# Performance work log

Measured on AMD Instinct MI355X. Metric: run time of the kernel, lower is better.

The kernel has to match this reference:

```python
import jax, jax.numpy as jnp
import numpy as np

GRID_SIZE = 5
GRID_LO, GRID_HI = -1.0, 1.0


def setup_inputs() -> dict:
    key = jax.random.key(0)
    k1, k2 = jax.random.split(key)
    B, out_dim, in_dim, H, W = 8, 64, 64, 192, 192
    G = GRID_SIZE + 1
    x = jax.random.normal(k1, (B, in_dim, H, W), dtype=jnp.float32)
    coef = jax.random.normal(k2, (B, out_dim, in_dim, G), dtype=jnp.float32) * 0.1
    return {"x": x, "coef": coef}


def reference(x, coef):
    # x: [B, in_dim, H, W]; coef: [B, out_dim, in_dim, G] with G = grid_size + 1
    G = GRID_SIZE + 1
    grid = jnp.linspace(GRID_LO, GRID_HI, G, dtype=x.dtype)
    lo, hi = grid[0], grid[-1]
    spacing = grid[1] - grid[0]

    B, in_dim, H, W = x.shape
    out_dim = coef.shape[1]
    P = H * W

    xf = x.reshape(B, in_dim, P)
    xc = jnp.clip(xf, lo, hi)
    nx = (xc - lo) / spacing                      # normalized coordinate in [0, grid_size]
    idx = jnp.clip(jnp.floor(nx).astype(jnp.int32), 0, GRID_SIZE - 1)  # left knot
    frac = nx - idx.astype(x.dtype)               # fractional offset (grad flows via nx)
    w1 = 1.0 - frac
    w2 = frac
    idx_next = jnp.clip(idx + 1, 0, GRID_SIZE)    # right knot (max index = G-1)

    # Two-hot interpolation weights over the G grid points: [B, in, P, G]
    Wt = (w1[..., None] * jax.nn.one_hot(idx, G, dtype=x.dtype)
          + w2[..., None] * jax.nn.one_hot(idx_next, G, dtype=x.dtype))

    # result[b,o,p] = sum_i sum_g Wt[b,i,p,g] * coef[b,o,i,g]
    out = jnp.einsum('bipg,boig->bop', Wt, coef)
    return out.reshape(B, out_dim, H, W)
```

## Files before the change

kernel.cpp:

```cpp
#include <hip/hip_runtime.h>
#include <stdint.h>


typedef __fp16 half8_t __attribute__((ext_vector_type(8)));
typedef __fp16 half2_t __attribute__((ext_vector_type(2)));
typedef float f32x4 __attribute__((ext_vector_type(4)));

#define NBATCH 8
#define OD 64
#define ID 64
#define PIX 36864
#define NG 6
#define PT 192
#define KI 16
#define NCHUNK 4
#define KC (KI * NG)
#define AROW 392
#define PTILES (PIX / PT)

__global__ __launch_bounds__(256, 3)
void kan_mfma(const float* __restrict__ x, const float* __restrict__ coef,
              float* __restrict__ out) {
  const int t = threadIdx.x;
  const int lane = t & 63;
  const int wave = t >> 6;
  const int q8 = lane >> 4;
  const int col = lane & 15;

  const int bid = blockIdx.x;
  const int b = bid / PTILES;
  const int ptile = bid % PTILES;
  const int p0 = ptile * PT;

  __shared__ __fp16 A_lds[OD][AROW] __attribute__((aligned(16)));

  {
    const int o = t >> 2;
    const int c = t & 3;
    const float* crow = coef + (size_t)b * (OD * ID * NG) + o * (ID * NG) + c * KC;
    __fp16* arow = &A_lds[o][c * KC];
#pragma unroll
    for (int blk = 0; blk < 8; ++blk) {
      f32x4 va = ((const f32x4*)crow)[blk * 3 + 0];
      f32x4 vb = ((const f32x4*)crow)[blk * 3 + 1];
      f32x4 vc = ((const f32x4*)crow)[blk * 3 + 2];
      const float lo[NG] = {va[0], va[1], va[2], va[3], vb[0], vb[1]};
      const float hi[NG] = {vb[2], vb[3], vc[0], vc[1], vc[2], vc[3]};
#pragma unroll
      for (int g = 0; g < NG; ++g) {
        half2_t h2 = __builtin_amdgcn_cvt_pkrtz(lo[g], hi[g]);
        *(half2_t*)&arow[g * KI + blk * 2] = h2;
      }
    }
  }

  f32x4 acc[4][3];
#pragma unroll
  for (int i = 0; i < 4; ++i)
#pragma unroll
    for (int j = 0; j < 3; ++j)
      acc[i][j] = (f32x4){0.f, 0.f, 0.f, 0.f};

  __syncthreads();

  const int iof0 = (q8 & 1) * 8;
  const int ghalf = q8 >> 1;
  const float* xb = x + (size_t)b * ID * PIX + p0 + wave * 48 + col
                      + (size_t)iof0 * PIX;

#pragma unroll
  for (int c = 0; c < NCHUNK; ++c) {
    const float* xs = xb + (size_t)(c * KI) * PIX;
    float nxv[3][8];
#pragma unroll
    for (int j = 0; j < 8; ++j) {
      const float* xj = xs + (size_t)j * PIX;
      float a0 = xj[0];
      float a1 = xj[16];
      float a2 = xj[32];
      nxv[0][j] = (fminf(fmaxf(a0, -1.f), 1.f) + 1.f) * 2.5f;
      nxv[1][j] = (fminf(fmaxf(a1, -1.f), 1.f) + 1.f) * 2.5f;
      nxv[2][j] = (fminf(fmaxf(a2, -1.f), 1.f) + 1.f) * 2.5f;
    }

#pragma unroll
    for (int ks = 0; ks < 3; ++ks) {
      half8_t af[4];
#pragma unroll
      for (int ot = 0; ot < 4; ++ot)
        af[ot] = *(const half8_t*)&A_lds[ot * 16 + col][c * KC + ks * 32 + q8 * 8];

      const float gf = (float)(2 * ks + ghalf);
#pragma unroll
      for (int pti = 0; pti < 3; ++pti) {
        union { half2_t h2[4]; half8_t v; } bu;
#pragma unroll
        for (int jj = 0; jj < 4; ++jj) {
          float h0 = fmaxf(0.f, 1.f - fabsf(nxv[pti][2 * jj] - gf));
          float h1 = fmaxf(0.f, 1.f - fabsf(nxv[pti][2 * jj + 1] - gf));
          bu.h2[jj] = __builtin_amdgcn_cvt_pkrtz(h0, h1);
        }
#pragma unroll
        for (int ot = 0; ot < 4; ++ot)
          acc[ot][pti] = __builtin_amdgcn_mfma_f32_16x16x32_f16(
              af[ot], bu.v, acc[ot][pti], 0, 0, 0);
      }
    }
  }

  float* ob = out + (size_t)b * OD * PIX + p0;
#pragma unroll
  for (int ot = 0; ot < 4; ++ot) {
#pragma unroll
    for (int pti = 0; pti < 3; ++pti) {
      int p = wave * 48 + pti * 16 + col;
#pragma unroll
      for (int r = 0; r < 4; ++r) {
        int o = ot * 16 + q8 * 4 + r;
        __builtin_nontemporal_store(acc[ot][pti][r], &ob[(size_t)o * PIX + p]);
      }
    }
  }
}

extern "C" void kernel_launch(void* const* d_in, const int* in_sizes, int n_in,
                              void* d_out, int out_size, void* d_ws, size_t ws_size,
                              hipStream_t stream) {
  const float* x = (const float*)d_in[0];
  const float* coef = (const float*)d_in[1];
  float* out = (float*)d_out;
  dim3 grid(NBATCH * PTILES);
  dim3 block(256);
  hipLaunchKernelGGL(kan_mfma, grid, block, 0, stream, x, coef, out);
}
```

Measured before the change: 161.2 us.

## Double-buffer x loads with inline asm and issue first chunk before coef staging

Issues the global loads for the first input chunk before the coefficient-to-LDS staging, then double-buffers the following chunks in registers using inline-asm loads and explicit vmcnt waits. The intent is to hide global-memory latency behind the LDS fill and the MFMA work. It also folds the clamp and normalize into one fma plus clamp, moves the hat-function max to a packed half2 max after conversion, and replaces nontemporal output stores with normal stores. The extra 48 registers per thread for the two buffers may put pressure on the 3-blocks-per-CU occupancy target.

Result: faster. 152.0 us (-5.7%).

```diff
diff --git a/kernel.cpp b/kernel.cpp
--- a/kernel.cpp
+++ b/kernel.cpp
@@ -18,6 +18,26 @@
 #define AROW 392
 #define PTILES (PIX / PT)
 
+#define LOADCHUNK(dst, cc)                                                      \
+  do {                                                                          \
+    _Pragma("unroll") for (int j = 0; j < 8; ++j) {                             \
+      const float* a_ = xb + (size_t)((cc) * KI + j) * PIX;                     \
+      asm volatile("global_load_dword %0, %3, off\n\t"                          \
+                   "global_load_dword %1, %3, off offset:64\n\t"                \
+                   "global_load_dword %2, %3, off offset:128"                   \
+                   : "=&v"(dst[j * 3 + 0]), "=&v"(dst[j * 3 + 1]),              \
+                     "=&v"(dst[j * 3 + 2])                                      \
+                   : "v"(a_));                                                  \
+    }                                                                           \
+    __builtin_amdgcn_sched_barrier(0);                                          \
+  } while (0)
+
+#define VMWAIT(n)                                                               \
+  do {                                                                          \
+    asm volatile("s_waitcnt vmcnt(" #n ")" ::: "memory");                       \
+    __builtin_amdgcn_sched_barrier(0);                                          \
+  } while (0)
+
 __global__ __launch_bounds__(256, 3)
 void kan_mfma(const float* __restrict__ x, const float* __restrict__ coef,
               float* __restrict__ out) {
@@ -33,6 +53,15 @@
   const int p0 = ptile * PT;
 
   __shared__ __fp16 A_lds[OD][AROW] __attribute__((aligned(16)));
+
+  const int iof0 = (q8 & 1) * 8;
+  const int ghalf = q8 >> 1;
+  const float* xb = x + (size_t)b * ID * PIX + p0 + wave * 48 + col
+                      + (size_t)iof0 * PIX;
+
+  float xA[24], xB[24];
+
+  LOADCHUNK(xA, 0);
 
   {
     const int o = t >> 2;
@@ -63,24 +92,24 @@
 
   __syncthreads();
 
-  const int iof0 = (q8 & 1) * 8;
-  const int ghalf = q8 >> 1;
-  const float* xb = x + (size_t)b * ID * PIX + p0 + wave * 48 + col
-                      + (size_t)iof0 * PIX;
-
 #pragma unroll
   for (int c = 0; c < NCHUNK; ++c) {
-    const float* xs = xb + (size_t)(c * KI) * PIX;
+    float* xc = (c & 1) ? xB : xA;
+    float* xn = (c & 1) ? xA : xB;
+
+    if (c + 1 < NCHUNK) {
+      LOADCHUNK(xn, c + 1);
+      VMWAIT(24);
+    } else {
+      VMWAIT(0);
+    }
+
     float nxv[3][8];
 #pragma unroll
     for (int j = 0; j < 8; ++j) {
-      const float* xj = xs + (size_t)j * PIX;
-      float a0 = xj[0];
-      float a1 = xj[16];
-      float a2 = xj[32];
-      nxv[0][j] = (fminf(fmaxf(a0, -1.f), 1.f) + 1.f) * 2.5f;
-      nxv[1][j] = (fminf(fmaxf(a1, -1.f), 1.f) + 1.f) * 2.5f;
-      nxv[2][j] = (fminf(fmaxf(a2, -1.f), 1.f) + 1.f) * 2.5f;
+#pragma unroll
+      for (int pt = 0; pt < 3; ++pt)
+        nxv[pt][j] = fminf(fmaxf(xc[j * 3 + pt] * 2.5f + 2.5f, 0.f), 5.f);
     }
 
 #pragma unroll
@@ -96,9 +125,10 @@
         union { half2_t h2[4]; half8_t v; } bu;
 #pragma unroll
         for (int jj = 0; jj < 4; ++jj) {
-          float h0 = fmaxf(0.f, 1.f - fabsf(nxv[pti][2 * jj] - gf));
-          float h1 = fmaxf(0.f, 1.f - fabsf(nxv[pti][2 * jj + 1] - gf));
-          bu.h2[jj] = __builtin_amdgcn_cvt_pkrtz(h0, h1);
+          float h0 = 1.f - fabsf(nxv[pti][2 * jj] - gf);
+          float h1 = 1.f - fabsf(nxv[pti][2 * jj + 1] - gf);
+          half2_t h2 = __builtin_amdgcn_cvt_pkrtz(h0, h1);
+          bu.h2[jj] = __builtin_elementwise_max(h2, (half2_t)(__fp16)0.f);
         }
 #pragma unroll
         for (int ot = 0; ot < 4; ++ot)
@@ -117,7 +147,7 @@
 #pragma unroll
       for (int r = 0; r < 4; ++r) {
         int o = ot * 16 + q8 * 4 + r;
-        __builtin_nontemporal_store(acc[ot][pti][r], &ob[(size_t)o * PIX + p]);
+        ob[(size_t)o * PIX + p] = acc[ot][pti][r];
       }
     }
   }
```

## Stage fp16 normalized inputs and output tile through LDS with vector accesses

Applied to the files above, without the earlier changes.

Each block now loads its x tile with coalesced float4 reads and converts it once to clamped normalized coordinates. These are packed as fp16 pairs into an LDS table that all waves read, replacing the strided per-lane scalar global loads and repeated normalization. The hat weights are computed with packed half2 arithmetic instead of fp32 followed by conversion. The output tile is staged through LDS, reusing the coefficient buffer, so stores are written as coalesced float4 nontemporal stores. Occupancy drops to two blocks per CU, extra barriers are added, and fp16 coordinates lower interpolation precision.

Result: faster. 149.6 us (-7.2%).

```diff
diff --git a/kernel.cpp b/kernel.cpp
--- a/kernel.cpp
+++ b/kernel.cpp
@@ -5,6 +5,7 @@
 typedef __fp16 half8_t __attribute__((ext_vector_type(8)));
 typedef __fp16 half2_t __attribute__((ext_vector_type(2)));
 typedef float f32x4 __attribute__((ext_vector_type(4)));
+typedef uint32_t u32x4 __attribute__((ext_vector_type(4)));
 
 #define NBATCH 8
 #define OD 64
@@ -16,9 +17,11 @@
 #define NCHUNK 4
 #define KC (KI * NG)
 #define AROW 392
+#define XSTR 196
+#define SROW 196
 #define PTILES (PIX / PT)
 
-__global__ __launch_bounds__(256, 3)
+__global__ __launch_bounds__(256, 2)
 void kan_mfma(const float* __restrict__ x, const float* __restrict__ coef,
               float* __restrict__ out) {
   const int t = threadIdx.x;
@@ -33,6 +36,15 @@
   const int p0 = ptile * PT;
 
   __shared__ __fp16 A_lds[OD][AROW] __attribute__((aligned(16)));
+  __shared__ uint32_t NX[2 * KI][XSTR] __attribute__((aligned(16)));
+
+  f32x4 xrow[16];
+  const float* xbase = x + (size_t)b * ID * PIX + p0;
+  if (lane < 48) {
+#pragma unroll
+    for (int k = 0; k < 16; ++k)
+      xrow[k] = *(const f32x4*)(xbase + (size_t)(wave * 16 + k) * PIX + lane * 4);
+  }
 
   {
     const int o = t >> 2;
@@ -54,6 +66,22 @@
     }
   }
 
+  if (lane < 48) {
+#pragma unroll
+    for (int pr = 0; pr < 8; ++pr) {
+      u32x4 w4;
+#pragma unroll
+      for (int j = 0; j < 4; ++j) {
+        float e = fminf(fmaxf(xrow[2 * pr][j] * 2.5f + 2.5f, 0.f), 5.f);
+        float o = fminf(fmaxf(xrow[2 * pr + 1][j] * 2.5f + 2.5f, 0.f), 5.f);
+        union { half2_t h; uint32_t u; } cv;
+        cv.h = __builtin_amdgcn_cvt_pkrtz(e, o);
+        w4[j] = cv.u;
+      }
+      *(u32x4*)&NX[wave * 8 + pr][lane * 4] = w4;
+    }
+  }
+
   f32x4 acc[4][3];
 #pragma unroll
   for (int i = 0; i < 4; ++i)
@@ -63,25 +91,20 @@
 
   __syncthreads();
 
-  const int iof0 = (q8 & 1) * 8;
   const int ghalf = q8 >> 1;
-  const float* xb = x + (size_t)b * ID * PIX + p0 + wave * 48 + col
-                      + (size_t)iof0 * PIX;
+  const int ipof = (q8 & 1) * 4;
+  const int wp = wave * 48 + col;
+  const half2_t one2 = {(__fp16)1.f, (__fp16)1.f};
+  const half2_t zero2 = {(__fp16)0.f, (__fp16)0.f};
 
 #pragma unroll
   for (int c = 0; c < NCHUNK; ++c) {
-    const float* xs = xb + (size_t)(c * KI) * PIX;
-    float nxv[3][8];
+    uint32_t nxp[3][4];
 #pragma unroll
-    for (int j = 0; j < 8; ++j) {
-      const float* xj = xs + (size_t)j * PIX;
-      float a0 = xj[0];
-      float a1 = xj[16];
-      float a2 = xj[32];
-      nxv[0][j] = (fminf(fmaxf(a0, -1.f), 1.f) + 1.f) * 2.5f;
-      nxv[1][j] = (fminf(fmaxf(a1, -1.f), 1.f) + 1.f) * 2.5f;
-      nxv[2][j] = (fminf(fmaxf(a2, -1.f), 1.f) + 1.f) * 2.5f;
-    }
+    for (int pti = 0; pti < 3; ++pti)
+#pragma unroll
+      for (int jj = 0; jj < 4; ++jj)
+        nxp[pti][jj] = NX[c * 8 + ipof + jj][wp + pti * 16];
 
 #pragma unroll
     for (int ks = 0; ks < 3; ++ks) {
@@ -90,15 +113,21 @@
       for (int ot = 0; ot < 4; ++ot)
         af[ot] = *(const half8_t*)&A_lds[ot * 16 + col][c * KC + ks * 32 + q8 * 8];
 
-      const float gf = (float)(2 * ks + ghalf);
+      const __fp16 gh = (__fp16)(float)(2 * ks + ghalf);
+      const half2_t gf2 = {gh, gh};
 #pragma unroll
       for (int pti = 0; pti < 3; ++pti) {
         union { half2_t h2[4]; half8_t v; } bu;
 #pragma unroll
         for (int jj = 0; jj < 4; ++jj) {
-          float h0 = fmaxf(0.f, 1.f - fabsf(nxv[pti][2 * jj] - gf));
-          float h1 = fmaxf(0.f, 1.f - fabsf(nxv[pti][2 * jj + 1] - gf));
-          bu.h2[jj] = __builtin_amdgcn_cvt_pkrtz(h0, h1);
+          union { uint32_t u; half2_t h; } nx;
+          nx.u = nxp[pti][jj];
+          half2_t d = nx.h - gf2;
+          union { half2_t h; uint32_t u; } du;
+          du.h = d;
+          du.u &= 0x7FFF7FFFu;
+          half2_t hh = one2 - du.h;
+          bu.h2[jj] = __builtin_elementwise_max(hh, zero2);
         }
 #pragma unroll
         for (int ot = 0; ot < 4; ++ot)
@@ -108,7 +137,8 @@
     }
   }
 
-  float* ob = out + (size_t)b * OD * PIX + p0;
+  __syncthreads();
+  float* S = (float*)&A_lds[0][0];
 #pragma unroll
   for (int ot = 0; ot < 4; ++ot) {
 #pragma unroll
@@ -117,8 +147,21 @@
 #pragma unroll
       for (int r = 0; r < 4; ++r) {
         int o = ot * 16 + q8 * 4 + r;
-        __builtin_nontemporal_store(acc[ot][pti][r], &ob[(size_t)o * PIX + p]);
+        S[o * SROW + p] = acc[ot][pti][r];
       }
+    }
+  }
+  __syncthreads();
+
+  {
+    float* ob = out + (size_t)b * OD * PIX + p0;
+#pragma unroll
+    for (int k = 0; k < 12; ++k) {
+      int flat = wave * 12288 + k * 1024 + lane * 16;
+      int row = flat / 768;
+      int colw = (flat - row * 768) >> 2;
+      f32x4 v = *(const f32x4*)&S[row * SROW + colw];
+      __builtin_nontemporal_store(v, (f32x4*)(ob + (size_t)row * PIX + colw));
     }
   }
 }
```
